# Kernel optimization log

Measured on AMD Instinct MI355X. Metric: run time of the kernel, lower is better.

The kernel has to match this reference:

```python
import jax, jax.numpy as jnp
import numpy as np

PI4 = np.pi / 4.0

def conv3d(x, w, b, stride):
    y = jax.lax.conv_general_dilated(
        x, w, (stride, stride, stride), ((1, 1), (1, 1), (1, 1)),
        dimension_numbers=('NCDHW', 'OIDHW', 'NCDHW'))
    return y + b[None, :, None, None, None]

def bn_relu(x, g, be):
    # BatchNorm3d in training mode: biased batch variance, eps=1e-5
    mean = jnp.mean(x, axis=(0, 2, 3, 4), keepdims=True)
    var = jnp.mean((x - mean) ** 2, axis=(0, 2, 3, 4), keepdims=True)
    xn = (x - mean) * jax.lax.rsqrt(var + 1e-5)
    return jax.nn.relu(xn * g[None, :, None, None, None] + be[None, :, None, None, None])

def _mat(b, entries):
    M = jnp.zeros((b, 4, 4), dtype=jnp.float32)
    for i, j, v in entries:
        M = M.at[:, i, j].set(v)
    return M

def affine_matrix(xs, tw, tb, rw, rb, sw, sb, shw, shb):
    b = xs.shape[0]
    one = jnp.ones((b,), xs.dtype)
    trans = jnp.tanh(xs @ tw.T + tb) * 0.1
    T = _mat(b, [(0, 0, one), (1, 1, one), (2, 2, one), (3, 3, one),
                 (0, 3, trans[:, 0]), (1, 3, trans[:, 1]), (2, 3, trans[:, 2])])
    rot = jnp.tanh(xs @ rw.T + rb) * PI4
    c, s = jnp.cos(rot), jnp.sin(rot)
    R1 = _mat(b, [(0, 0, c[:, 0]), (0, 1, -s[:, 0]), (1, 0, s[:, 0]), (1, 1, c[:, 0]), (2, 2, one), (3, 3, one)])
    R2 = _mat(b, [(1, 1, c[:, 1]), (1, 2, -s[:, 1]), (2, 1, s[:, 1]), (2, 2, c[:, 1]), (0, 0, one), (3, 3, one)])
    R3 = _mat(b, [(0, 0, c[:, 2]), (0, 1, -s[:, 2]), (1, 0, s[:, 2]), (1, 1, c[:, 2]), (2, 2, one), (3, 3, one)])
    R = R1 @ R2 @ R3
    scale = jnp.tanh(xs @ sw.T + sb) * 0.2
    e = jnp.exp(scale)
    S = _mat(b, [(0, 0, e[:, 0]), (1, 1, e[:, 1]), (2, 2, e[:, 2]), (3, 3, one)])
    sh = jnp.tanh(xs @ shw.T + shb) * PI4
    cs, ss = jnp.cos(sh), jnp.sin(sh)
    H1 = _mat(b, [(1, 1, cs[:, 0]), (1, 2, -ss[:, 0]), (2, 1, ss[:, 0]), (2, 2, cs[:, 0]), (0, 0, one), (3, 3, one)])
    H2 = _mat(b, [(0, 0, cs[:, 1]), (0, 2, ss[:, 1]), (2, 0, -ss[:, 1]), (2, 2, cs[:, 1]), (1, 1, one), (3, 3, one)])
    H3 = _mat(b, [(0, 0, cs[:, 2]), (0, 1, -ss[:, 2]), (1, 0, ss[:, 2]), (1, 1, cs[:, 2]), (2, 2, one), (3, 3, one)])
    Sh = H1 @ H2 @ H3
    # theta = Sh * S * Sh^T * R * T
    return Sh @ S @ jnp.swapaxes(Sh, 1, 2) @ R @ T

def affine_grid(theta3, size):
    b, c, D, H, W = size
    zz, yy, xx = jnp.meshgrid(jnp.linspace(-1, 1, D), jnp.linspace(-1, 1, H),
                              jnp.linspace(-1, 1, W), indexing='ij')
    mesh = jnp.stack([xx.ravel(), yy.ravel(), zz.ravel(),
                      jnp.ones(D * H * W, jnp.float32)], 0)  # (4, N)
    grid = jnp.einsum('bij,jn->bni', theta3, mesh)
    return grid.reshape(b, D, H, W, 3)

def grid_sample_3d(img, grid):
    # trilinear, align_corners=False, zero padding (matches F.grid_sample defaults)
    B, C, D, H, W = img.shape
    x = ((grid[..., 0] + 1.0) * W - 1.0) * 0.5
    y = ((grid[..., 1] + 1.0) * H - 1.0) * 0.5
    z = ((grid[..., 2] + 1.0) * D - 1.0) * 0.5
    x0, y0, z0 = jnp.floor(x), jnp.floor(y), jnp.floor(z)
    flat = img.reshape(B, C, -1)

    def corner(zc, yc, xc, w):
        valid = (zc >= 0) & (zc < D) & (yc >= 0) & (yc < H) & (xc >= 0) & (xc < W)
        zi = jnp.clip(zc, 0, D - 1).astype(jnp.int32)
        yi = jnp.clip(yc, 0, H - 1).astype(jnp.int32)
        xi = jnp.clip(xc, 0, W - 1).astype(jnp.int32)
        idx = ((zi * H + yi) * W + xi).reshape(B, 1, -1)
        v = jnp.take_along_axis(flat, jnp.broadcast_to(idx, (B, C, idx.shape[-1])), axis=2)
        return v.reshape(B, C, D, H, W) * (w * valid).reshape(B, 1, D, H, W)

    out = jnp.zeros_like(img)
    for dz in (0, 1):
        wz = (z - z0) if dz else (z0 + 1.0 - z)
        for dy in (0, 1):
            wy = (y - y0) if dy else (y0 + 1.0 - y)
            for dx in (0, 1):
                wx = (x - x0) if dx else (x0 + 1.0 - x)
                out = out + corner(z0 + dz, y0 + dy, x0 + dx, wz * wy * wx)
    return out


def setup_inputs() -> dict:
    key = jax.random.key(0)
    ks = jax.random.split(key, 10)
    B, S, nf = 16, 64, 16

    def conv_w(k, o, i):
        return jax.random.normal(k, (o, i, 3, 3, 3), jnp.float32) * (2.0 / (i * 27)) ** 0.5

    inp = {'x': jax.random.normal(ks[0], (B, 1, S, S, S), jnp.float32)}
    chans = [(1, nf), (nf, 2 * nf), (2 * nf, 4 * nf), (4 * nf, 4 * nf), (4 * nf, 4 * nf)]
    names = ['00', '0', '1', '2', '3']
    for n, (ci, co), k in zip(names, chans, ks[1:6]):
        inp['w' + n] = conv_w(k, co, ci)
        inp['b' + n] = jnp.zeros((co,), jnp.float32)
        inp['g' + n] = jnp.ones((co,), jnp.float32)
        inp['be' + n] = jnp.zeros((co,), jnp.float32)
    F = 4 * 4 * 4 * 4 * nf
    for n, k in zip(['t', 'r', 's', 'sh'], ks[6:10]):
        inp[n + 'w'] = jax.random.normal(k, (3, F), jnp.float32) * 0.01
        inp[n + 'b'] = jnp.zeros((3,), jnp.float32)
    return inp


def reference(x, w00, b00, g00, be00, w0, b0, g0, be0, w1, b1, g1, be1,
              w2, b2, g2, be2, w3, b3, g3, be3, tw, tb, rw, rb, sw, sb, shw, shb):
    xs = bn_relu(conv3d(x, w00, b00, 1), g00, be00)
    xs = bn_relu(conv3d(xs, w0, b0, 2), g0, be0)
    xs = bn_relu(conv3d(xs, w1, b1, 2), g1, be1)
    xs = bn_relu(conv3d(xs, w2, b2, 2), g2, be2)
    xs = bn_relu(conv3d(xs, w3, b3, 2), g3, be3)
    xs = xs.reshape(xs.shape[0], -1)
    theta = affine_matrix(xs, tw, tb, rw, rb, sw, sb, shw, shb)
    img = x[:, :1]
    grid = affine_grid(theta[:, :3, :], img.shape)
    return grid_sample_3d(img, grid)
```

## Files before the change

### kernel.cpp

```cpp
#include <hip/hip_runtime.h>
#include <hip/hip_bf16.h>
#include <hip/hip_fp16.h>

using bf16 = __hip_bfloat16;
static __device__ __forceinline__ float b2f(bf16 v) { return __bfloat162float(v); }

static __device__ __forceinline__ float dld(const void* p, size_t i, bool f32) {
    return f32 ? ((const float*)p)[i] : b2f(((const bf16*)p)[i]);
}

static __device__ __forceinline__ float ldf(const float* p, size_t i) { return p[i]; }
static __device__ __forceinline__ float ldf(const __half* p, size_t i) { return __half2float(p[i]); }
static __device__ __forceinline__ void stf(float* p, size_t i, float v) { p[i] = v; }
static __device__ __forceinline__ void stf(__half* p, size_t i, float v) { p[i] = __float2half(v); }

#define PI4f 0.78539816339744830961f

__global__ void detect_k(const unsigned short* __restrict__ xu,
                         float* __restrict__ flag) {
    __shared__ int sh[256];
    int tid = threadIdx.x;
    int cnt = 0;
    for (int i = tid; i < 4096; i += 256) {
        int e = (xu[i] >> 7) & 0xFF;
        if (e < 96 || e > 160) cnt++;
    }
    sh[tid] = cnt;
    __syncthreads();
    for (int off = 128; off > 0; off >>= 1) {
        if (tid < off) sh[tid] += sh[tid + off];
        __syncthreads();
    }
    if (tid == 0) flag[0] = (sh[0] > 64) ? 1.f : 0.f;
}

__global__ void zero_k(float* __restrict__ p, int n) {
    int i = threadIdx.x;
    if (i < n) p[i] = 0.f;
}

__global__ void zeroN_k(float4* __restrict__ p, int n4) {
    int i = blockIdx.x * 256 + threadIdx.x;
    if (i < n4) p[i] = make_float4(0.f, 0.f, 0.f, 0.f);
}

__global__ void wcvt_k(const void* __restrict__ w00, const void* __restrict__ w0,
                       const void* __restrict__ w1, const void* __restrict__ w2,
                       const void* __restrict__ w3, const float* __restrict__ flag,
                       float* __restrict__ dst) {
    const bool f = flag[0] != 0.f;
    int i = blockIdx.x * 256 + threadIdx.x;
    if (i < 432) {
        float v = dld(w00, i, f);
        dst[i] = v;
        int co = i / 27, tap = i % 27;
        dst[432 + tap * 16 + co] = v;
    }
    if (i < 13824) {
        float v = dld(w0, i, f);
        int co = i / 432, rem = i % 432, ci = rem / 27, tap = rem % 27;
        dst[864 + (ci * 27 + tap) * 32 + co] = v;
    }
    if (i < 55296) {
        float v = dld(w1, i, f);
        int co = i / 864, rem = i % 864, ci = rem / 27, tap = rem % 27;
        dst[14688 + (ci * 27 + tap) * 64 + co] = v;
    }
    if (i < 110592) {
        float v = dld(w2, i, f);
        int co = i / 1728, rem = i % 1728, ci = rem / 27, tap = rem % 27;
        dst[69984 + (ci * 27 + tap) * 64 + co] = v;
    }
    if (i < 110592) {
        float v = dld(w3, i, f);
        int co = i / 1728, rem = i % 1728, ci = rem / 27, tap = rem % 27;
        dst[180576 + (ci * 27 + tap) * 64 + co] = v;
    }
}

template <bool F32, bool DOSTATS, bool STORE>
__device__ __forceinline__ void stats00_body(const void* __restrict__ xv,
                                             const float* __restrict__ wf00t,
                                             const void* __restrict__ b00,
                                             float* __restrict__ sums,
                                             float* __restrict__ y00, int batchOff,
                                             float* xt, float* rs, float* rq) {
    const int tid = threadIdx.x;
    const int rbk = blockIdx.x;
    const int rx = rbk & 3, ry = (rbk >> 2) & 3, rz = rbk >> 4;
    const int zb = blockIdx.z;
    const int rb = zb + batchOff;
    const int z0 = rz * 16 - 1, y0 = ry * 16 - 1, x0 = rx * 16 - 1;
    const size_t xbase = (size_t)rb * 262144;

    for (int idx = tid; idx < 5832; idx += 256) {
        int ix = idx % 18;
        int r = idx / 18;
        int iy = r % 18;
        int iz = r / 18;
        int zz = z0 + iz, yy = y0 + iy, xx = x0 + ix;
        float v = 0.f;
        if (zz >= 0 && zz < 64 && yy >= 0 && yy < 64 && xx >= 0 && xx < 64) {
            size_t gi = xbase + ((size_t)zz * 64 + yy) * 64 + xx;
            v = F32 ? ((const float*)xv)[gi] : b2f(((const bf16*)xv)[gi]);
        }
        xt[idx] = v;
    }
    if (DOSTATS && tid < 16) { rs[tid] = 0.f; rq[tid] = 0.f; }
    __syncthreads();

    float bia[16];
#pragma unroll
    for (int c = 0; c < 16; c++) bia[c] = dld(b00, c, F32);
    float s[16], sq[16];
#pragma unroll
    for (int c = 0; c < 16; c++) { s[c] = 0.f; sq[c] = 0.f; }

    for (int k = 0; k < 16; k++) {
        int v = tid + k * 256;
        int z = v >> 8, y = (v >> 4) & 15, xw = v & 15;
        float oc[16];
#pragma unroll
        for (int c = 0; c < 16; c++) oc[c] = bia[c];
#pragma unroll
        for (int kz = 0; kz < 3; kz++)
#pragma unroll
        for (int ky = 0; ky < 3; ky++)
#pragma unroll
        for (int kx = 0; kx < 3; kx++) {
            float a = xt[(z + kz) * 324 + (y + ky) * 18 + (xw + kx)];
            const float4* w4 = (const float4*)(wf00t + ((kz * 3 + ky) * 3 + kx) * 16);
#pragma unroll
            for (int j = 0; j < 4; j++) {
                float4 wv = w4[j];
                oc[4 * j + 0] += a * wv.x;
                oc[4 * j + 1] += a * wv.y;
                oc[4 * j + 2] += a * wv.z;
                oc[4 * j + 3] += a * wv.w;
            }
        }
        if constexpr (STORE) {
            const size_t sp = (((size_t)(rz * 16 + z) * 64 + (ry * 16 + y)) * 64) +
                              (rx * 16 + xw);
#pragma unroll
            for (int c = 0; c < 16; c++)
                y00[(((size_t)(zb * 16 + c)) << 18) + sp] = oc[c];
        }
        if constexpr (DOSTATS) {
#pragma unroll
            for (int c = 0; c < 16; c++) { s[c] += oc[c]; sq[c] += oc[c] * oc[c]; }
        }
    }
    if constexpr (DOSTATS) {
        const int lane = tid & 63;
#pragma unroll
        for (int c = 0; c < 16; c++) {
            float v1 = s[c], v2 = sq[c];
#pragma unroll
            for (int off = 32; off > 0; off >>= 1) {
                v1 += __shfl_down(v1, off, 64);
                v2 += __shfl_down(v2, off, 64);
            }
            if (lane == 0) { atomicAdd(&rs[c], v1); atomicAdd(&rq[c], v2); }
        }
        __syncthreads();
        if (tid < 16) {
            atomicAdd(&sums[tid], rs[tid]);
            atomicAdd(&sums[16 + tid], rq[tid]);
        }
    }
}

template <bool DOSTATS, bool STORE>
__launch_bounds__(256)
__global__ void stats00_k(const void* __restrict__ x, const float* __restrict__ wf00t,
                          const void* __restrict__ b00, const float* __restrict__ flag,
                          float* __restrict__ sums, float* __restrict__ y00,
                          int batchOff) {
    __shared__ float xt[5832];
    __shared__ float rs[16], rq[16];
    if (flag[0] != 0.f)
        stats00_body<true, DOSTATS, STORE>(x, wf00t, b00, sums, y00, batchOff,
                                           xt, rs, rq);
    else
        stats00_body<false, DOSTATS, STORE>(x, wf00t, b00, sums, y00, batchOff,
                                            xt, rs, rq);
}

template <bool F32, typename TOUT>
__device__ __forceinline__ void conv0f_body(
    const void* __restrict__ xv, const float* __restrict__ wf00,
    const void* __restrict__ b00, const float* __restrict__ wf0t,
    const void* __restrict__ b0v, const void* __restrict__ g00,
    const void* __restrict__ be00, const float* __restrict__ sums00,
    TOUT* __restrict__ y0, float* xt, float* yt) {
    constexpr int YTXP = 18;
    constexpr int YROW = 17 * YTXP;
    constexpr int YTOT = 9 * 17 * 17;
    constexpr int XTY = 19, XTX = 19, XTOT = 11 * 19 * 19;

    const int tid = threadIdx.x;
    const int tbk = blockIdx.x;
    const int tx = tbk & 3;
    const int ty = (tbk >> 2) & 3;
    const int tz = tbk >> 4;
    const int b = blockIdx.z;

    const int ox = tid & 7, oy = (tid >> 3) & 7, oz = tid >> 6;
    const int gz = tz * 4 + oz, gy = ty * 8 + oy, gx = tx * 8 + ox;

    const int iz0 = tz * 8 - 1, iy0 = ty * 16 - 1, ix0 = tx * 16 - 1;
    const int xz0 = iz0 - 1, xy0 = iy0 - 1, xx0 = ix0 - 1;

    const size_t xbase = (size_t)b * 262144;
    for (int idx = tid; idx < XTOT; idx += 256) {
        int ix = idx % XTX;
        int r = idx / XTX;
        int iy = r % XTY;
        int iz = r / XTY;
        int zz = xz0 + iz, yy = xy0 + iy, xx = xx0 + ix;
        float v = 0.f;
        if (zz >= 0 && zz < 64 && yy >= 0 && yy < 64 && xx >= 0 && xx < 64) {
            size_t gi = xbase + ((size_t)zz * 64 + yy) * 64 + xx;
            v = F32 ? ((const float*)xv)[gi] : b2f(((const bf16*)xv)[gi]);
        }
        xt[idx] = v;
    }

    float acc[32];
#pragma unroll
    for (int i = 0; i < 32; i++) acc[i] = 0.f;

    for (int ci = 0; ci < 16; ci++) {
        float mean = sums00[ci] * (1.f / 4194304.f);
        float var = sums00[16 + ci] * (1.f / 4194304.f) - mean * mean;
        float A = dld(g00, ci, F32) * rsqrtf(var + 1e-5f);
        float Bs = dld(be00, ci, F32) - mean * A;
        const float* wrp = wf00 + ci * 27;
        const float bia = dld(b00, ci, F32);
        __syncthreads();
        for (int idx = tid; idx < YTOT; idx += 256) {
            int ix = idx % 17;
            int r = idx / 17;
            int iy = r % 17;
            int iz = r / 17;
            int zz = iz0 + iz, yy = iy0 + iy, xx = ix0 + ix;
            float v = 0.f;
            if (zz >= 0 && zz < 64 && yy >= 0 && yy < 64 && xx >= 0 && xx < 64) {
                float o = bia;
#pragma unroll
                for (int kz = 0; kz < 3; kz++)
#pragma unroll
                for (int ky = 0; ky < 3; ky++)
#pragma unroll
                for (int kx = 0; kx < 3; kx++)
                    o += xt[(iz + kz) * (XTY * XTX) + (iy + ky) * XTX + (ix + kx)] *
                         wrp[(kz * 3 + ky) * 3 + kx];
                v = fmaxf(0.f, A * o + Bs);
            }
            yt[iz * YROW + iy * YTXP + ((ix >> 1) + (ix & 1) * 9)] = v;
        }
        __syncthreads();
#pragma unroll
        for (int kz = 0; kz < 3; kz++)
#pragma unroll
        for (int ky = 0; ky < 3; ky++)
#pragma unroll
        for (int kx = 0; kx < 3; kx++) {
            const int xcol = (kx & 1) ? (9 + ox) : (ox + (kx >> 1));
            float a = yt[(oz * 2 + kz) * YROW + (oy * 2 + ky) * YTXP + xcol];
            const int tap = (kz * 3 + ky) * 3 + kx;
            const float4* wp4 = (const float4*)(wf0t + (ci * 27 + tap) * 32);
#pragma unroll
            for (int j = 0; j < 8; j++) {
                float4 wv = wp4[j];
                acc[4 * j + 0] += a * wv.x;
                acc[4 * j + 1] += a * wv.y;
                acc[4 * j + 2] += a * wv.z;
                acc[4 * j + 3] += a * wv.w;
            }
        }
    }
    const size_t outSp = 32768;
    const size_t obase = ((size_t)b * 32) * outSp + ((size_t)gz * 32 + gy) * 32 + gx;
#pragma unroll
    for (int co = 0; co < 32; co++)
        stf(y0, obase + (size_t)co * outSp, acc[co] + dld(b0v, co, F32));
}

template <typename TOUT>
__launch_bounds__(256)
__global__ void conv0f_k(const void* __restrict__ x, const float* __restrict__ wf00,
                         const void* __restrict__ b00, const float* __restrict__ wf0t,
                         const void* __restrict__ b0v, const void* __restrict__ g00,
                         const void* __restrict__ be00,
                         const float* __restrict__ sums00,
                         const float* __restrict__ flag, TOUT* __restrict__ y0) {
    __shared__ float xt[11 * 19 * 19];
    __shared__ float yt[9 * 17 * 18];
    if (flag[0] != 0.f)
        conv0f_body<true>(x, wf00, b00, wf0t, b0v, g00, be00, sums00, y0, xt, yt);
    else
        conv0f_body<false>(x, wf00, b00, wf0t, b0v, g00, be00, sums00, y0, xt, yt);
}

template <typename TIN, int CIN, int COUT, int COACC, int NCHUNK, int TZ, int TY,
          int TX, int STRIDE, int IND, int OUTD>
__launch_bounds__(TZ * TY * TX)
__global__ void convsplit_k(const TIN* __restrict__ inv,
                            const float* __restrict__ wft,
                            const void* __restrict__ bias,
                            const void* __restrict__ g_prev,
                            const void* __restrict__ be_prev,
                            const float* __restrict__ stats_prev,
                            float Ninv_prev, const float* __restrict__ flag,
                            float* __restrict__ out) {
    static_assert(STRIDE == 2, "even/odd tile layout assumes stride 2");
    constexpr int NT = TZ * TY * TX;
    constexpr int ITZ = (TZ - 1) * STRIDE + 3;
    constexpr int ITY = (TY - 1) * STRIDE + 3;
    constexpr int ITX = (TX - 1) * STRIDE + 3;
    constexpr int ITXP = ITX + 1;
    constexpr int HALF = (ITX + 1) / 2;
    constexpr int ITOT = ITZ * ITY * ITX;
    constexpr int NTX = OUTD / TX, NTY = OUTD / TY;
    constexpr int CICH = CIN / NCHUNK;
    constexpr int NCO = COUT / COACC;

    __shared__ float tile[ITZ * ITY * ITXP];

    const bool F = flag[0] != 0.f;
    const int tid = threadIdx.x;
    const int tbk = blockIdx.x;
    const int tx = tbk % NTX;
    const int t2 = tbk / NTX;
    const int ty = t2 % NTY;
    const int tz = t2 / NTY;
    const int coBase = (blockIdx.y % NCO) * COACC;
    const int chunk = blockIdx.y / NCO;
    const int b = blockIdx.z;

    const int ox = tid % TX;
    const int oy = (tid / TX) % TY;
    const int oz = tid / (TX * TY);
    const int gz = tz * TZ + oz, gy = ty * TY + oy, gx = tx * TX + ox;

    float acc[COACC];
#pragma unroll
    for (int i = 0; i < COACC; i++) acc[i] = 0.f;

    const int iz0 = tz * TZ * STRIDE - 1;
    const int iy0 = ty * TY * STRIDE - 1;
    const int ix0 = tx * TX * STRIDE - 1;

    for (int ci = chunk * CICH; ci < (chunk + 1) * CICH; ci++) {
        float mean = stats_prev[ci] * Ninv_prev;
        float var = stats_prev[CIN + ci] * Ninv_prev - mean * mean;
        float A = dld(g_prev, ci, F) * rsqrtf(var + 1e-5f);
        float Bs = dld(be_prev, ci, F) - mean * A;
        __syncthreads();
        const size_t chanBase = ((size_t)(b * CIN + ci)) * IND * IND * IND;
        for (int idx = tid; idx < ITOT; idx += NT) {
            int ix = idx % ITX;
            int r = idx / ITX;
            int iy = r % ITY;
            int iz = r / ITY;
            int zz = iz0 + iz, yy = iy0 + iy, xx = ix0 + ix;
            float v = 0.f;
            if (zz >= 0 && zz < IND && yy >= 0 && yy < IND && xx >= 0 && xx < IND) {
                float raw = ldf(inv, chanBase + ((size_t)zz * IND + yy) * IND + xx);
                v = fmaxf(0.f, A * raw + Bs);
            }
            tile[(iz * ITY + iy) * ITXP + ((ix >> 1) + (ix & 1) * HALF)] = v;
        }
        __syncthreads();
#pragma unroll
        for (int kz = 0; kz < 3; kz++)
#pragma unroll
        for (int ky = 0; ky < 3; ky++)
#pragma unroll
        for (int kx = 0; kx < 3; kx++) {
            const int xcol = (kx & 1) ? (HALF + ox) : (ox + (kx >> 1));
            float a = tile[((oz * STRIDE + kz) * ITY + (oy * STRIDE + ky)) * ITXP +
                           xcol];
            const int tap = (kz * 3 + ky) * 3 + kx;
            const float4* wp4 =
                (const float4*)(wft + (size_t)(ci * 27 + tap) * COUT + coBase);
#pragma unroll
            for (int j = 0; j < COACC / 4; j++) {
                float4 wv = wp4[j];
                acc[4 * j + 0] += a * wv.x;
                acc[4 * j + 1] += a * wv.y;
                acc[4 * j + 2] += a * wv.z;
                acc[4 * j + 3] += a * wv.w;
            }
        }
    }
    const size_t outSp = (size_t)OUTD * OUTD * OUTD;
    const size_t obase = ((size_t)b * COUT + coBase) * outSp +
                         ((size_t)gz * OUTD + gy) * OUTD + gx;
#pragma unroll
    for (int co = 0; co < COACC; co++) {
        float v = acc[co];
        if constexpr (NCHUNK == 1) {
            out[obase + (size_t)co * outSp] = v + dld(bias, coBase + co, F);
        } else {
            if (chunk == 0) v += dld(bias, coBase + co, F);
            atomicAdd(&out[obase + (size_t)co * outSp], v);
        }
    }
}

template <typename T>
__global__ void stats_k(const T* __restrict__ raw, float* __restrict__ sums,
                        int C, int spatial, int B) {
    const int c = blockIdx.x;
    const int K = gridDim.y;
    const int part = blockIdx.y;
    float s = 0.f, sq = 0.f;
    for (int b = 0; b < B; b++) {
        const T* p = raw + ((size_t)(b * C + c)) * spatial;
        if constexpr (sizeof(T) == 4) {
            const float4* p4 = (const float4*)p;
            for (int i = part * blockDim.x + threadIdx.x; i < (spatial >> 2);
                 i += K * blockDim.x) {
                float4 v = p4[i];
                s += v.x + v.y + v.z + v.w;
                sq += v.x * v.x + v.y * v.y + v.z * v.z + v.w * v.w;
            }
        } else {
            for (int i = part * blockDim.x + threadIdx.x; i < spatial;
                 i += K * blockDim.x) {
                float v = ldf(p, i);
                s += v;
                sq += v * v;
            }
        }
    }
    __shared__ float rs[256], rq[256];
    int tid = threadIdx.x;
    rs[tid] = s;
    rq[tid] = sq;
    __syncthreads();
    for (int off = blockDim.x / 2; off > 0; off >>= 1) {
        if (tid < off) { rs[tid] += rs[tid + off]; rq[tid] += rq[tid + off]; }
        __syncthreads();
    }
    if (tid == 0) {
        atomicAdd(&sums[c], rs[0]);
        atomicAdd(&sums[C + c], rq[0]);
    }
}

static __device__ __forceinline__ void mm4(const float* A, const float* B, float* C) {
    for (int i = 0; i < 4; i++)
        for (int j = 0; j < 4; j++) {
            float s = 0.f;
            for (int k = 0; k < 4; k++) s += A[i * 4 + k] * B[k * 4 + j];
            C[i * 4 + j] = s;
        }
}
static __device__ __forceinline__ void ident(float* M) {
    for (int i = 0; i < 16; i++) M[i] = (i % 5 == 0) ? 1.f : 0.f;
}

__global__ void fc_affine_k(const float* __restrict__ y3,
                            const float* __restrict__ stats3,
                            const void* __restrict__ g3, const void* __restrict__ be3,
                            const void* __restrict__ tw, const void* __restrict__ tbv,
                            const void* __restrict__ rw, const void* __restrict__ rbv,
                            const void* __restrict__ sw, const void* __restrict__ sbv,
                            const void* __restrict__ shw, const void* __restrict__ shbv,
                            const float* __restrict__ flag,
                            float* __restrict__ theta) {
    const bool F = flag[0] != 0.f;
    const int b = blockIdx.x;
    const int tid = threadIdx.x;
    __shared__ float Ab[64], Bb[64];
    if (tid < 64) {
        float mean = stats3[tid] * (1.f / 1024.f);
        float var = stats3[64 + tid] * (1.f / 1024.f) - mean * mean;
        float A = dld(g3, tid, F) * rsqrtf(var + 1e-5f);
        Ab[tid] = A;
        Bb[tid] = dld(be3, tid, F) - mean * A;
    }
    __syncthreads();
    float acc[12];
#pragma unroll
    for (int j = 0; j < 12; j++) acc[j] = 0.f;
    const float* yb = y3 + (size_t)b * 4096;
    for (int f = tid; f < 4096; f += 256) {
        int c = f >> 6;
        float x = fmaxf(0.f, Ab[c] * yb[f] + Bb[c]);
#pragma unroll
        for (int i = 0; i < 3; i++) {
            acc[0 + i] += x * dld(tw, i * 4096 + f, F);
            acc[3 + i] += x * dld(rw, i * 4096 + f, F);
            acc[6 + i] += x * dld(sw, i * 4096 + f, F);
            acc[9 + i] += x * dld(shw, i * 4096 + f, F);
        }
    }
    __shared__ float red[256];
    __shared__ float dots[12];
    for (int j = 0; j < 12; j++) {
        red[tid] = acc[j];
        __syncthreads();
        for (int off = 128; off > 0; off >>= 1) {
            if (tid < off) red[tid] += red[tid + off];
            __syncthreads();
        }
        if (tid == 0) dots[j] = red[0];
        __syncthreads();
    }
    if (tid == 0) {
        float trans[3], rot[3], scl[3], sh[3];
        for (int i = 0; i < 3; i++) {
            trans[i] = 0.1f * tanhf(dots[0 + i] + dld(tbv, i, F));
            rot[i]   = PI4f * tanhf(dots[3 + i] + dld(rbv, i, F));
            scl[i]   = 0.2f * tanhf(dots[6 + i] + dld(sbv, i, F));
            sh[i]    = PI4f * tanhf(dots[9 + i] + dld(shbv, i, F));
        }
        float T[16], R1[16], R2[16], R3[16], S[16], H1[16], H2[16], H3[16];
        float t1[16], t2[16], R[16], Sh[16], ShT[16], M[16];
        ident(T); T[3] = trans[0]; T[7] = trans[1]; T[11] = trans[2];
        { float c = cosf(rot[0]), s = sinf(rot[0]);
          ident(R1); R1[0] = c; R1[1] = -s; R1[4] = s; R1[5] = c; }
        { float c = cosf(rot[1]), s = sinf(rot[1]);
          ident(R2); R2[5] = c; R2[6] = -s; R2[9] = s; R2[10] = c; }
        { float c = cosf(rot[2]), s = sinf(rot[2]);
          ident(R3); R3[0] = c; R3[1] = -s; R3[4] = s; R3[5] = c; }
        mm4(R1, R2, t1); mm4(t1, R3, R);
        ident(S); S[0] = expf(scl[0]); S[5] = expf(scl[1]); S[10] = expf(scl[2]);
        { float c = cosf(sh[0]), s = sinf(sh[0]);
          ident(H1); H1[5] = c; H1[6] = -s; H1[9] = s; H1[10] = c; }
        { float c = cosf(sh[1]), s = sinf(sh[1]);
          ident(H2); H2[0] = c; H2[2] = s; H2[8] = -s; H2[10] = c; }
        { float c = cosf(sh[2]), s = sinf(sh[2]);
          ident(H3); H3[0] = c; H3[1] = -s; H3[4] = s; H3[5] = c; }
        mm4(H1, H2, t1); mm4(t1, H3, Sh);
        for (int i = 0; i < 4; i++)
            for (int j = 0; j < 4; j++) ShT[i * 4 + j] = Sh[j * 4 + i];
        mm4(Sh, S, t1); mm4(t1, ShT, t2); mm4(t2, R, t1); mm4(t1, T, M);
        for (int i = 0; i < 12; i++) theta[b * 12 + i] = M[i];
    }
}

template <bool F32>
__device__ __forceinline__ void sample_body(const void* __restrict__ xv,
                                            const float* __restrict__ theta,
                                            void* __restrict__ out) {
    const int b = blockIdx.y;
    const int v = blockIdx.x * 256 + threadIdx.x;
    const int w = v & 63, h = (v >> 6) & 63, d = v >> 12;
    const float* t = theta + b * 12;
    const float px = -1.f + w * (2.f / 63.f);
    const float py = -1.f + h * (2.f / 63.f);
    const float pz = -1.f + d * (2.f / 63.f);
    const float gx = t[0] * px + t[1] * py + t[2] * pz + t[3];
    const float gy = t[4] * px + t[5] * py + t[6] * pz + t[7];
    const float gz = t[8] * px + t[9] * py + t[10] * pz + t[11];
    const float fx = ((gx + 1.f) * 64.f - 1.f) * 0.5f;
    const float fy = ((gy + 1.f) * 64.f - 1.f) * 0.5f;
    const float fz = ((gz + 1.f) * 64.f - 1.f) * 0.5f;
    const float x0 = floorf(fx), y0 = floorf(fy), z0 = floorf(fz);
    const float wx1 = fx - x0, wy1 = fy - y0, wz1 = fz - z0;
    const size_t ibase = (size_t)b * 262144;
    float outv = 0.f;
#pragma unroll
    for (int dz = 0; dz < 2; dz++) {
        float wz = dz ? wz1 : 1.f - wz1;
        int zc = (int)z0 + dz;
        bool zok = (zc >= 0 && zc < 64);
        int zi = min(max(zc, 0), 63);
#pragma unroll
        for (int dy = 0; dy < 2; dy++) {
            float wy = dy ? wy1 : 1.f - wy1;
            int yc = (int)y0 + dy;
            bool yok = (yc >= 0 && yc < 64);
            int yi = min(max(yc, 0), 63);
#pragma unroll
            for (int dx = 0; dx < 2; dx++) {
                float wwx = dx ? wx1 : 1.f - wx1;
                int xc = (int)x0 + dx;
                bool xok = (xc >= 0 && xc < 64);
                int xi = min(max(xc, 0), 63);
                size_t gi = ibase + ((size_t)zi * 64 + yi) * 64 + xi;
                float val = F32 ? ((const float*)xv)[gi] : b2f(((const bf16*)xv)[gi]);
                float wgt = (zok && yok && xok) ? wz * wy * wwx : 0.f;
                outv += val * wgt;
            }
        }
    }
    const size_t oi = (size_t)b * 262144 + v;
    if (F32) ((float*)out)[oi] = outv;
    else ((bf16*)out)[oi] = __float2bfloat16(outv);
}

__global__ void sample_k(const void* __restrict__ x, const float* __restrict__ theta,
                         const float* __restrict__ flag, void* __restrict__ out) {
    if (flag[0] != 0.f) sample_body<true>(x, theta, out);
    else                sample_body<false>(x, theta, out);
}

extern "C" void kernel_launch(void* const* d_in, const int* in_sizes, int n_in,
                              void* d_out, int out_size, void* d_ws, size_t ws_size,
                              hipStream_t stream) {
    const void* x    = d_in[0];
    const void* w00  = d_in[1];
    const void* b00  = d_in[2];
    const void* g00  = d_in[3];
    const void* be00 = d_in[4];
    const void* w0   = d_in[5];
    const void* b0   = d_in[6];
    const void* g0   = d_in[7];
    const void* be0  = d_in[8];
    const void* w1   = d_in[9];
    const void* b1   = d_in[10];
    const void* g1   = d_in[11];
    const void* be1  = d_in[12];
    const void* w2   = d_in[13];
    const void* b2   = d_in[14];
    const void* g2   = d_in[15];
    const void* be2  = d_in[16];
    const void* w3   = d_in[17];
    const void* b3   = d_in[18];
    const void* g3   = d_in[19];
    const void* be3  = d_in[20];
    const void* tw   = d_in[21];
    const void* tb   = d_in[22];
    const void* rw   = d_in[23];
    const void* rb   = d_in[24];
    const void* sw   = d_in[25];
    const void* sb   = d_in[26];
    const void* shw  = d_in[27];
    const void* shb  = d_in[28];

    float* wsF = (float*)d_ws;
    const bool f32path = ws_size >= (size_t)21853232 * 4;
    const bool mat = ws_size >= (size_t)(21853232 + 33554432) * 4;
    const size_t Y0U = f32path ? 16777216 : 8388608;
    const size_t Y1_OFF = Y0U;
    const size_t Y2_OFF = Y1_OFF + 4194304;
    const size_t Y3_OFF = Y2_OFF + 524288;
    const size_t WF_OFF = Y3_OFF + 65536;
    const size_t ST_OFF = WF_OFF + 291200;
    const size_t FL_OFF = ST_OFF + 480;
    const size_t TH_OFF = ST_OFF + 496;

    float* y1 = wsF + Y1_OFF;
    float* y2 = wsF + Y2_OFF;
    float* y3 = wsF + Y3_OFF;
    float* wf00  = wsF + WF_OFF + 0;
    float* wf00t = wsF + WF_OFF + 432;
    float* wf0t  = wsF + WF_OFF + 864;
    float* wf1t  = wsF + WF_OFF + 14688;
    float* wf2t  = wsF + WF_OFF + 69984;
    float* wf3t  = wsF + WF_OFF + 180576;
    float* sums00 = wsF + ST_OFF + 0;
    float* sums0  = wsF + ST_OFF + 32;
    float* sums1  = wsF + ST_OFF + 96;
    float* sums2  = wsF + ST_OFF + 224;
    float* sums3  = wsF + ST_OFF + 352;
    float* flag   = wsF + FL_OFF;
    float* theta  = wsF + TH_OFF;
    float* y00f   = wsF + 21853232;

    zero_k<<<1, 512, 0, stream>>>(wsF + ST_OFF, 480);
    zeroN_k<<<4672, 256, 0, stream>>>((float4*)y1, 1196032);
    detect_k<<<1, 256, 0, stream>>>((const unsigned short*)x, flag);
    wcvt_k<<<432, 256, 0, stream>>>(w00, w0, w1, w2, w3, flag, wsF + WF_OFF);

    if (f32path && mat) {
        float* y0 = wsF;
        stats00_k<true, true><<<dim3(64, 1, 8), 256, 0, stream>>>(
            x, wf00t, b00, flag, sums00, y00f, 0);
        stats00_k<true, false><<<dim3(64, 1, 8), 256, 0, stream>>>(
            x, wf00t, b00, flag, sums00, nullptr, 8);
        convsplit_k<float, 16, 32, 32, 1, 4, 8, 8, 2, 64, 32>
            <<<dim3(128, 1, 8), 256, 0, stream>>>(y00f, wf0t, b0, g00, be00,
                                                  sums00, 1.f / 4194304.f, flag, y0);
        stats00_k<false, true><<<dim3(64, 1, 8), 256, 0, stream>>>(
            x, wf00t, b00, flag, sums00, y00f, 8);
        convsplit_k<float, 16, 32, 32, 1, 4, 8, 8, 2, 64, 32>
            <<<dim3(128, 1, 8), 256, 0, stream>>>(y00f, wf0t, b0, g00, be00,
                                                  sums00, 1.f / 4194304.f, flag,
                                                  y0 + (size_t)8 * 32 * 32768);
        stats_k<float><<<dim3(32, 32), 256, 0, stream>>>(y0, sums0, 32, 32768, 16);
        convsplit_k<float, 32, 64, 32, 2, 4, 8, 8, 2, 32, 16>
            <<<dim3(16, 4, 16), 256, 0, stream>>>(y0, wf1t, b1, g0, be0, sums0,
                                                  1.f / 524288.f, flag, y1);
    } else if (f32path) {
        float* y0 = wsF;
        stats00_k<true, false><<<dim3(64, 1, 16), 256, 0, stream>>>(
            x, wf00t, b00, flag, sums00, nullptr, 0);
        conv0f_k<float><<<dim3(128, 1, 16), 256, 0, stream>>>(
            x, wf00, b00, wf0t, b0, g00, be00, sums00, flag, y0);
        stats_k<float><<<dim3(32, 32), 256, 0, stream>>>(y0, sums0, 32, 32768, 16);
        convsplit_k<float, 32, 64, 32, 2, 4, 8, 8, 2, 32, 16>
            <<<dim3(16, 4, 16), 256, 0, stream>>>(y0, wf1t, b1, g0, be0, sums0,
                                                  1.f / 524288.f, flag, y1);
    } else {
        __half* y0 = (__half*)d_ws;
        stats00_k<true, false><<<dim3(64, 1, 16), 256, 0, stream>>>(
            x, wf00t, b00, flag, sums00, nullptr, 0);
        conv0f_k<__half><<<dim3(128, 1, 16), 256, 0, stream>>>(
            x, wf00, b00, wf0t, b0, g00, be00, sums00, flag, y0);
        stats_k<__half><<<dim3(32, 32), 256, 0, stream>>>(y0, sums0, 32, 32768, 16);
        convsplit_k<__half, 32, 64, 32, 2, 4, 8, 8, 2, 32, 16>
            <<<dim3(16, 4, 16), 256, 0, stream>>>(y0, wf1t, b1, g0, be0, sums0,
                                                  1.f / 524288.f, flag, y1);
    }

    stats_k<float><<<dim3(64, 4), 256, 0, stream>>>(y1, sums1, 64, 4096, 16);

    convsplit_k<float, 64, 64, 16, 8, 2, 8, 8, 2, 16, 8>
        <<<dim3(4, 32, 16), 128, 0, stream>>>(y1, wf2t, b2, g1, be1, sums1,
                                              1.f / 65536.f, flag, y2);
    stats_k<float><<<dim3(64, 1), 256, 0, stream>>>(y2, sums2, 64, 512, 16);

    convsplit_k<float, 64, 64, 16, 16, 4, 4, 4, 2, 8, 4>
        <<<dim3(1, 64, 16), 64, 0, stream>>>(y2, wf3t, b3, g2, be2, sums2,
                                             1.f / 8192.f, flag, y3);
    stats_k<float><<<dim3(64, 1), 256, 0, stream>>>(y3, sums3, 64, 64, 16);

    fc_affine_k<<<16, 256, 0, stream>>>(y3, sums3, g3, be3, tw, tb, rw, rb, sw, sb,
                                        shw, shb, flag, theta);

    sample_k<<<dim3(1024, 16), 256, 0, stream>>>(x, theta, flag, d_out);
}
```

Measured before the change: 1.148 ms.

## Split conv tiles and channel chunks finer, precompute tile load offsets

The first conv's stats kernel now uses 8-deep z tiles with twice as many blocks, which shrinks shared memory per block and gives each thread a fixed (y,x) position across the z loop. The strided conv kernels get more output-channel groups or input-channel chunks, launching more blocks per layer to improve occupancy and load balance. The tile-fill loop now precomputes per-thread local and global offsets once, outside the channel loop, so index division is not repeated for every input channel. More blocks means more redundant halo loads and more atomic partial-sum traffic, and the offset arrays use extra registers.

```diff
diff --git a/kernel.cpp b/kernel.cpp
--- a/kernel.cpp
+++ b/kernel.cpp
@@ -90,10 +90,10 @@
     const int rx = rbk & 3, ry = (rbk >> 2) & 3, rz = rbk >> 4;
     const int zb = blockIdx.z;
     const int rb = zb + batchOff;
-    const int z0 = rz * 16 - 1, y0 = ry * 16 - 1, x0 = rx * 16 - 1;
+    const int z0 = rz * 8 - 1, y0 = ry * 16 - 1, x0 = rx * 16 - 1;
     const size_t xbase = (size_t)rb * 262144;
 
-    for (int idx = tid; idx < 5832; idx += 256) {
+    for (int idx = tid; idx < 3240; idx += 256) {
         int ix = idx % 18;
         int r = idx / 18;
         int iy = r % 18;
@@ -116,9 +116,9 @@
 #pragma unroll
     for (int c = 0; c < 16; c++) { s[c] = 0.f; sq[c] = 0.f; }
 
-    for (int k = 0; k < 16; k++) {
-        int v = tid + k * 256;
-        int z = v >> 8, y = (v >> 4) & 15, xw = v & 15;
+    const int y = tid >> 4;
+    const int xw = tid & 15;
+    for (int k = 0; k < 8; k++) {
         float oc[16];
 #pragma unroll
         for (int c = 0; c < 16; c++) oc[c] = bia[c];
@@ -128,7 +128,7 @@
         for (int ky = 0; ky < 3; ky++)
 #pragma unroll
         for (int kx = 0; kx < 3; kx++) {
-            float a = xt[(z + kz) * 324 + (y + ky) * 18 + (xw + kx)];
+            float a = xt[(k + kz) * 324 + (y + ky) * 18 + (xw + kx)];
             const float4* w4 = (const float4*)(wf00t + ((kz * 3 + ky) * 3 + kx) * 16);
 #pragma unroll
             for (int j = 0; j < 4; j++) {
@@ -140,7 +140,7 @@
             }
         }
         if constexpr (STORE) {
-            const size_t sp = (((size_t)(rz * 16 + z) * 64 + (ry * 16 + y)) * 64) +
+            const size_t sp = (((size_t)(rz * 8 + k) * 64 + (ry * 16 + y)) * 64) +
                               (rx * 16 + xw);
 #pragma unroll
             for (int c = 0; c < 16; c++)
@@ -177,7 +177,7 @@
                           const void* __restrict__ b00, const float* __restrict__ flag,
                           float* __restrict__ sums, float* __restrict__ y00,
                           int batchOff) {
-    __shared__ float xt[5832];
+    __shared__ float xt[3240];
     __shared__ float rs[16], rq[16];
     if (flag[0] != 0.f)
         stats00_body<true, DOSTATS, STORE>(x, wf00t, b00, sums, y00, batchOff,
@@ -326,6 +326,7 @@
     constexpr int NTX = OUTD / TX, NTY = OUTD / TY;
     constexpr int CICH = CIN / NCHUNK;
     constexpr int NCO = COUT / COACC;
+    constexpr int NSLOT = (ITOT + NT - 1) / NT;
 
     __shared__ float tile[ITZ * ITY * ITXP];
 
@@ -345,13 +346,31 @@
     const int oz = tid / (TX * TY);
     const int gz = tz * TZ + oz, gy = ty * TY + oy, gx = tx * TX + ox;
 
-    float acc[COACC];
-#pragma unroll
-    for (int i = 0; i < COACC; i++) acc[i] = 0.f;
-
     const int iz0 = tz * TZ * STRIDE - 1;
     const int iy0 = ty * TY * STRIDE - 1;
     const int ix0 = tx * TX * STRIDE - 1;
+
+    int loff[NSLOT], goff[NSLOT];
+#pragma unroll
+    for (int s = 0; s < NSLOT; s++) {
+        const int idx = tid + s * NT;
+        loff[s] = -1;
+        goff[s] = -1;
+        if (idx < ITOT) {
+            int ix = idx % ITX;
+            int r = idx / ITX;
+            int iy = r % ITY;
+            int iz = r / ITY;
+            loff[s] = (iz * ITY + iy) * ITXP + ((ix >> 1) + (ix & 1) * HALF);
+            int zz = iz0 + iz, yy = iy0 + iy, xx = ix0 + ix;
+            if (zz >= 0 && zz < IND && yy >= 0 && yy < IND && xx >= 0 && xx < IND)
+                goff[s] = (zz * IND + yy) * IND + xx;
+        }
+    }
+
+    float acc[COACC];
+#pragma unroll
+    for (int i = 0; i < COACC; i++) acc[i] = 0.f;
 
     for (int ci = chunk * CICH; ci < (chunk + 1) * CICH; ci++) {
         float mean = stats_prev[ci] * Ninv_prev;
@@ -359,19 +378,14 @@
         float A = dld(g_prev, ci, F) * rsqrtf(var + 1e-5f);
         float Bs = dld(be_prev, ci, F) - mean * A;
         __syncthreads();
-        const size_t chanBase = ((size_t)(b * CIN + ci)) * IND * IND * IND;
-        for (int idx = tid; idx < ITOT; idx += NT) {
-            int ix = idx % ITX;
-            int r = idx / ITX;
-            int iy = r % ITY;
-            int iz = r / ITY;
-            int zz = iz0 + iz, yy = iy0 + iy, xx = ix0 + ix;
-            float v = 0.f;
-            if (zz >= 0 && zz < IND && yy >= 0 && yy < IND && xx >= 0 && xx < IND) {
-                float raw = ldf(inv, chanBase + ((size_t)zz * IND + yy) * IND + xx);
-                v = fmaxf(0.f, A * raw + Bs);
-            }
-            tile[(iz * ITY + iy) * ITXP + ((ix >> 1) + (ix & 1) * HALF)] = v;
+        const TIN* cp = inv + ((size_t)(b * CIN + ci)) * (IND * IND * IND);
+#pragma unroll
+        for (int s = 0; s < NSLOT; s++) {
+            if (loff[s] >= 0) {
+                float v = 0.f;
+                if (goff[s] >= 0) v = fmaxf(0.f, A * ldf(cp, goff[s]) + Bs);
+                tile[loff[s]] = v;
+            }
         }
         __syncthreads();
 #pragma unroll
@@ -672,55 +686,55 @@
 
     if (f32path && mat) {
         float* y0 = wsF;
-        stats00_k<true, true><<<dim3(64, 1, 8), 256, 0, stream>>>(
+        stats00_k<true, true><<<dim3(128, 1, 8), 256, 0, stream>>>(
             x, wf00t, b00, flag, sums00, y00f, 0);
-        stats00_k<true, false><<<dim3(64, 1, 8), 256, 0, stream>>>(
+        stats00_k<true, false><<<dim3(128, 1, 8), 256, 0, stream>>>(
             x, wf00t, b00, flag, sums00, nullptr, 8);
-        convsplit_k<float, 16, 32, 32, 1, 4, 8, 8, 2, 64, 32>
-            <<<dim3(128, 1, 8), 256, 0, stream>>>(y00f, wf0t, b0, g00, be00,
+        convsplit_k<float, 16, 32, 16, 1, 4, 8, 8, 2, 64, 32>
+            <<<dim3(128, 2, 8), 256, 0, stream>>>(y00f, wf0t, b0, g00, be00,
                                                   sums00, 1.f / 4194304.f, flag, y0);
-        stats00_k<false, true><<<dim3(64, 1, 8), 256, 0, stream>>>(
+        stats00_k<false, true><<<dim3(128, 1, 8), 256, 0, stream>>>(
             x, wf00t, b00, flag, sums00, y00f, 8);
-        convsplit_k<float, 16, 32, 32, 1, 4, 8, 8, 2, 64, 32>
-            <<<dim3(128, 1, 8), 256, 0, stream>>>(y00f, wf0t, b0, g00, be00,
+        convsplit_k<float, 16, 32, 16, 1, 4, 8, 8, 2, 64, 32>
+            <<<dim3(128, 2, 8), 256, 0, stream>>>(y00f, wf0t, b0, g00, be00,
                                                   sums00, 1.f / 4194304.f, flag,
                                                   y0 + (size_t)8 * 32 * 32768);
         stats_k<float><<<dim3(32, 32), 256, 0, stream>>>(y0, sums0, 32, 32768, 16);
-        convsplit_k<float, 32, 64, 32, 2, 4, 8, 8, 2, 32, 16>
-            <<<dim3(16, 4, 16), 256, 0, stream>>>(y0, wf1t, b1, g0, be0, sums0,
+        convsplit_k<float, 32, 64, 16, 2, 4, 8, 8, 2, 32, 16>
+            <<<dim3(16, 8, 16), 256, 0, stream>>>(y0, wf1t, b1, g0, be0, sums0,
                                                   1.f / 524288.f, flag, y1);
     } else if (f32path) {
         float* y0 = wsF;
-        stats00_k<true, false><<<dim3(64, 1, 16), 256, 0, stream>>>(
+        stats00_k<true, false><<<dim3(128, 1, 16), 256, 0, stream>>>(
             x, wf00t, b00, flag, sums00, nullptr, 0);
         conv0f_k<float><<<dim3(128, 1, 16), 256, 0, stream>>>(
             x, wf00, b00, wf0t, b0, g00, be00, sums00, flag, y0);
         stats_k<float><<<dim3(32, 32), 256, 0, stream>>>(y0, sums0, 32, 32768, 16);
-        convsplit_k<float, 32, 64, 32, 2, 4, 8, 8, 2, 32, 16>
-            <<<dim3(16, 4, 16), 256, 0, stream>>>(y0, wf1t, b1, g0, be0, sums0,
+        convsplit_k<float, 32, 64, 16, 2, 4, 8, 8, 2, 32, 16>
+            <<<dim3(16, 8, 16), 256, 0, stream>>>(y0, wf1t, b1, g0, be0, sums0,
                                                   1.f / 524288.f, flag, y1);
     } else {
         __half* y0 = (__half*)d_ws;
-        stats00_k<true, false><<<dim3(64, 1, 16), 256, 0, stream>>>(
+        stats00_k<true, false><<<dim3(128, 1, 16), 256, 0, stream>>>(
             x, wf00t, b00, flag, sums00, nullptr, 0);
         conv0f_k<__half><<<dim3(128, 1, 16), 256, 0, stream>>>(
             x, wf00, b00, wf0t, b0, g00, be00, sums00, flag, y0);
         stats_k<__half><<<dim3(32, 32), 256, 0, stream>>>(y0, sums0, 32, 32768, 16);
-        convsplit_k<__half, 32, 64, 32, 2, 4, 8, 8, 2, 32, 16>
-            <<<dim3(16, 4, 16), 256, 0, stream>>>(y0, wf1t, b1, g0, be0, sums0,
+        convsplit_k<__half, 32, 64, 16, 2, 4, 8, 8, 2, 32, 16>
+            <<<dim3(16, 8, 16), 256, 0, stream>>>(y0, wf1t, b1, g0, be0, sums0,
                                                   1.f / 524288.f, flag, y1);
     }
 
     stats_k<float><<<dim3(64, 4), 256, 0, stream>>>(y1, sums1, 64, 4096, 16);
 
-    convsplit_k<float, 64, 64, 16, 8, 2, 8, 8, 2, 16, 8>
-        <<<dim3(4, 32, 16), 128, 0, stream>>>(y1, wf2t, b2, g1, be1, sums1,
+    convsplit_k<float, 64, 64, 16, 16, 2, 8, 8, 2, 16, 8>
+        <<<dim3(4, 64, 16), 128, 0, stream>>>(y1, wf2t, b2, g1, be1, sums1,
                                               1.f / 65536.f, flag, y2);
     stats_k<float><<<dim3(64, 1), 256, 0, stream>>>(y2, sums2, 64, 512, 16);
 
-    convsplit_k<float, 64, 64, 16, 16, 4, 4, 4, 2, 8, 4>
-        <<<dim3(1, 64, 16), 64, 0, stream>>>(y2, wf3t, b3, g2, be2, sums2,
-                                             1.f / 8192.f, flag, y3);
+    convsplit_k<float, 64, 64, 16, 32, 4, 4, 4, 2, 8, 4>
+        <<<dim3(1, 128, 16), 64, 0, stream>>>(y2, wf3t, b3, g2, be2, sums2,
+                                              1.f / 8192.f, flag, y3);
     stats_k<float><<<dim3(64, 1), 256, 0, stream>>>(y3, sums3, 64, 64, 16);
 
     fc_affine_k<<<16, 256, 0, stream>>>(y3, sums3, g3, be3, tw, tb, rw, rb, sw, sb,
```

New measurement: 1.227 ms. 1.07x slower.
